# Kernel tuning notes

Hardware: AMD Instinct MI355X
Metric: run time of the kernel (lower is better)

The kernel has to match this reference:

```python
import jax, jax.numpy as jnp
import numpy as np

N_NODES = 100000
AVG_DEG = 32
E_UND = N_NODES * AVG_DEG // 2   # 1.6M undirected edges
E_DIR = 2 * E_UND                # 3.2M directed edges
Q = 4                            # number of communities
NUM_ITER = 10                    # max_num_iter in bp_params


def setup_inputs() -> dict:
    key = jax.random.key(0)
    k1, k2, k3, k4 = jax.random.split(key, 4)
    src_u = jax.random.randint(k1, (E_UND,), 0, N_NODES)
    dst_u = jax.random.randint(k2, (E_UND,), 0, N_NODES)
    # symmetric directed edge list: [forward block | reverse block]
    edge_index = jnp.stack([
        jnp.concatenate([src_u, dst_u]),
        jnp.concatenate([dst_u, src_u]),
    ]).astype(jnp.int64)
    w_u = jax.random.uniform(k3, (E_UND,), dtype=jnp.float32)
    edge_attr = jnp.concatenate([w_u, w_u])  # symmetric weights
    msg_init = jax.random.uniform(k4, (E_DIR, Q), dtype=jnp.float32) + 0.1
    # critical beta for q groups, mean degree c: log(q/(sqrt(c)-1)+1)
    beta = jnp.asarray(np.log(Q / (np.sqrt(AVG_DEG) - 1.0) + 1.0), dtype=jnp.float32)
    return {"edge_index": edge_index, "edge_attr": edge_attr,
            "msg_init": msg_init, "beta": beta, "num_nodes": N_NODES}


def _bp_forward(edge_index, edge_attr, msg_init, beta, num_nodes):
    q = msg_init.shape[1]
    E = edge_index.shape[1]
    e_und = E // 2
    src, dst = edge_index[0], edge_index[1]
    # reverse-edge permutation: edge e <-> e +/- e_und
    rev = jnp.concatenate([jnp.arange(e_und) + e_und, jnp.arange(e_und)])

    two_m = jnp.sum(edge_attr)                                   # = 2m (directed sum)
    deg = jax.ops.segment_sum(edge_attr, src, num_segments=num_nodes)  # weighted degree [N]
    expm1_bw = jnp.expm1(beta * edge_attr)[:, None]              # [E,1]

    psi0 = msg_init / jnp.sum(msg_init, axis=-1, keepdims=True)  # normalized cavity msgs [E,q]
    h0 = jnp.zeros((q,), dtype=msg_init.dtype)                   # external field

    def step(carry, _):
        psi, h = carry
        L = jnp.log1p(psi * expm1_bw)                            # [E,q] log(1 + psi*(e^{bw}-1))
        S = jax.ops.segment_sum(L, dst, num_segments=num_nodes)  # [N,q] incoming log-products
        marg = jax.nn.softmax(h[None, :] + S, axis=-1)           # node marginals [N,q]
        h_new = -(beta / two_m) * jnp.sum(deg[:, None] * marg, axis=0)  # [q]
        # cavity update for edge i->j: all incoming at i except reverse edge j->i
        msg_log = h_new[None, :] + S[src] - L[rev]
        psi_new = jax.nn.softmax(msg_log, axis=-1)
        return (psi_new, h_new), None

    (psi, h), _ = jax.lax.scan(step, (psi0, h0), None, length=NUM_ITER)

    # final node marginals s
    L = jnp.log1p(psi * expm1_bw)
    S = jax.ops.segment_sum(L, dst, num_segments=num_nodes)
    s = jax.nn.softmax(h[None, :] + S, axis=-1)                  # [N,q]

    # modularity: Q = (1/2m) sum_e w_e <s_i, s_j> - sum_t (sum_i d_i s_it / 2m)^2
    link = jnp.sum(edge_attr[:, None] * s[src] * s[dst]) / two_m
    comm_deg = jnp.sum(deg[:, None] * s, axis=0) / two_m         # [q]
    q_mod = link - jnp.sum(comm_deg * comm_deg)
    return s, q_mod


def reference(edge_index, edge_attr, msg_init, beta, num_nodes):
    return _bp_forward(edge_index, edge_attr, msg_init, beta, num_nodes)
```

## Files before the change

kernel.cpp:

```cpp
#include <hip/hip_runtime.h>


#define NBLK 256
#define QD 4
#define SENT 0x7fffffff

__device__ __forceinline__ float wave_red(float v) {
#pragma unroll
  for (int o = 32; o > 0; o >>= 1) v += __shfl_down(v, o, 64);
  return v;
}

__device__ __forceinline__ float4 softmax4(float a, float b, float c, float d) {
  float mx = fmaxf(fmaxf(a, b), fmaxf(c, d));
  float e0 = expf(a - mx), e1 = expf(b - mx), e2 = expf(c - mx), e3 = expf(d - mx);
  float inv = 1.f / (e0 + e1 + e2 + e3);
  return make_float4(e0 * inv, e1 * inv, e2 * inv, e3 * inv);
}

__global__ void hist_rank(const int* __restrict__ ei, int* __restrict__ cnt,
                          int* __restrict__ rank, int E) {
  int G = gridDim.x * blockDim.x;
  int e0 = blockIdx.x * blockDim.x + threadIdx.x;
  int e1 = e0 + G, e2 = e0 + 2 * G, e3 = e0 + 3 * G;
  int d0 = (e0 < E) ? ei[E + e0] : 0;
  int d1 = (e1 < E) ? ei[E + e1] : 0;
  int d2 = (e2 < E) ? ei[E + e2] : 0;
  int d3 = (e3 < E) ? ei[E + e3] : 0;
  if (e0 < E) rank[e0] = atomicAdd(&cnt[d0], 1);
  if (e1 < E) rank[e1] = atomicAdd(&cnt[d1], 1);
  if (e2 < E) rank[e2] = atomicAdd(&cnt[d2], 1);
  if (e3 < E) rank[e3] = atomicAdd(&cnt[d3], 1);
}

__global__ void scanA(const int* __restrict__ cnt, int* __restrict__ out,
                      int* __restrict__ bsum, int N) {
  __shared__ int lds[256];
  int base = blockIdx.x * 1024 + threadIdx.x * 4;
  int v0 = (base + 0 < N) ? cnt[base + 0] : 0;
  int v1 = (base + 1 < N) ? cnt[base + 1] : 0;
  int v2 = (base + 2 < N) ? cnt[base + 2] : 0;
  int v3 = (base + 3 < N) ? cnt[base + 3] : 0;
  lds[threadIdx.x] = v0 + v1 + v2 + v3;
  __syncthreads();
  for (int off = 1; off < 256; off <<= 1) {
    int x = (threadIdx.x >= off) ? lds[threadIdx.x - off] : 0;
    __syncthreads();
    if (threadIdx.x >= off) lds[threadIdx.x] += x;
    __syncthreads();
  }
  int excl = (threadIdx.x == 0) ? 0 : lds[threadIdx.x - 1];
  if (threadIdx.x == 255) bsum[blockIdx.x] = lds[255];
  if (base + 0 < N) out[base + 0] = excl;
  if (base + 1 < N) out[base + 1] = excl + v0;
  if (base + 2 < N) out[base + 2] = excl + v0 + v1;
  if (base + 3 < N) out[base + 3] = excl + v0 + v1 + v2;
}

__global__ void scanB(int* __restrict__ bsum, int NB) {
  __shared__ int lds[256];
  int v = (threadIdx.x < NB) ? bsum[threadIdx.x] : 0;
  lds[threadIdx.x] = v;
  __syncthreads();
  for (int off = 1; off < 256; off <<= 1) {
    int x = (threadIdx.x >= off) ? lds[threadIdx.x - off] : 0;
    __syncthreads();
    if (threadIdx.x >= off) lds[threadIdx.x] += x;
    __syncthreads();
  }
  int excl = (threadIdx.x == 0) ? 0 : lds[threadIdx.x - 1];
  if (threadIdx.x < NB) bsum[threadIdx.x] = excl;
}

__global__ void scanC(int* __restrict__ rowStart, const int* __restrict__ bsum,
                      int N, int E) {
  int i = blockIdx.x * blockDim.x + threadIdx.x;
  if (i < N) rowStart[i] += bsum[i >> 10];
  if (i == 0) rowStart[N] = E;
}

__global__ void scatter_inc(const int* __restrict__ ei, const int* __restrict__ rowStart,
                            const int* __restrict__ rank, int* __restrict__ inc, int E) {
  int e = blockIdx.x * blockDim.x + threadIdx.x;
  if (e >= E) return;
  int d = ei[E + e];
  inc[rowStart[d] + rank[e]] = e;
}

__global__ void build_nodeOf(const int* __restrict__ rowStart, int* __restrict__ nodeOf,
                             int N) {
  int n = blockIdx.x * blockDim.x + threadIdx.x;
  if (n >= N) return;
  int s = rowStart[n], e = rowStart[n + 1];
  for (int k = s; k < e; ++k) nodeOf[k] = n;
}

__global__ void reduce_w(const float* __restrict__ w, double* __restrict__ two_m, int E) {
  __shared__ float blk[4];
  int G = gridDim.x * blockDim.x;
  float acc = 0.f;
  for (int i = blockIdx.x * blockDim.x + threadIdx.x; i < E; i += G) acc += w[i];
  acc = wave_red(acc);
  int wid = threadIdx.x >> 6;
  if ((threadIdx.x & 63) == 0) blk[wid] = acc;
  __syncthreads();
  if (threadIdx.x == 0)
    atomicAdd(two_m, (double)(blk[0] + blk[1] + blk[2] + blk[3]));
}

__global__ void setup_pairs(const float* __restrict__ w, const float* __restrict__ msg,
                            const float* __restrict__ beta_p, float* __restrict__ L,
                            float* __restrict__ em_buf, int Eh) {
  int t = blockIdx.x * blockDim.x + threadIdx.x;
  if (t >= Eh) return;
  float beta = beta_p[0];
  float wv = w[t];
  float em = expm1f(beta * wv);
  em_buf[t] = em;
  float4 m1 = *reinterpret_cast<const float4*>(&msg[(size_t)t * QD]);
  float4 m2 = *reinterpret_cast<const float4*>(&msg[((size_t)t + Eh) * QD]);
  float i1 = 1.f / (m1.x + m1.y + m1.z + m1.w);
  float i2 = 1.f / (m2.x + m2.y + m2.z + m2.w);
  float4 L1 = make_float4(log1pf(m1.x * i1 * em), log1pf(m1.y * i1 * em),
                          log1pf(m1.z * i1 * em), log1pf(m1.w * i1 * em));
  float4 L2 = make_float4(log1pf(m2.x * i2 * em), log1pf(m2.y * i2 * em),
                          log1pf(m2.z * i2 * em), log1pf(m2.w * i2 * em));
  *reinterpret_cast<float4*>(&L[(size_t)t * QD]) = L1;
  *reinterpret_cast<float4*>(&L[((size_t)t + Eh) * QD]) = L2;
}

template <int NC>
__global__ void gather_seg(const int* __restrict__ inc, const int* __restrict__ nodeOf,
                           const float* __restrict__ src, float* __restrict__ out,
                           int E) {
  const int lane = threadIdx.x & 63;
  const int wid = threadIdx.x >> 6;
  const long long base = ((long long)blockIdx.x * (blockDim.x >> 6) + wid) * 256;
  if (base >= E) return;
  int n[4], idx[4];
  float v[4][NC];
#pragma unroll
  for (int w = 0; w < 4; ++w) {
    long long k = base + w * 64 + lane;
    n[w] = (k < E) ? nodeOf[k] : SENT;
    idx[w] = (k < E) ? inc[k] : 0;
  }
#pragma unroll
  for (int w = 0; w < 4; ++w) {
    long long k = base + w * 64 + lane;
    if (k < E) {
      if constexpr (NC == 4) {
        float4 t = *reinterpret_cast<const float4*>(&src[(size_t)idx[w] * 4]);
        v[w][0] = t.x; v[w][1] = t.y; v[w][2] = t.z; v[w][3] = t.w;
      } else {
        v[w][0] = src[idx[w]];
      }
    } else {
#pragma unroll
      for (int c = 0; c < NC; ++c) v[w][c] = 0.f;
    }
  }
  int n00 = __shfl(n[0], 0, 64);
  int prevn = (base > 0) ? nodeOf[base - 1] : -1;
  const int incomplete = (prevn == n00) ? n00 : -1;
  int nwf[4];
#pragma unroll
  for (int w = 0; w < 3; ++w) nwf[w] = __shfl(n[w + 1], 0, 64);
  nwf[3] = (base + 256 < E) ? nodeOf[base + 256] : -1;

  float cv[NC];
#pragma unroll
  for (int c = 0; c < NC; ++c) cv[c] = 0.f;
  int cn = -1;
#pragma unroll
  for (int w = 0; w < 4; ++w) {
    int nn = n[w];
#pragma unroll
    for (int d = 1; d < 64; d <<= 1) {
      int pn = __shfl_up(nn, d, 64);
      float pv[NC];
#pragma unroll
      for (int c = 0; c < NC; ++c) pv[c] = __shfl_up(v[w][c], d, 64);
      if (lane >= d && pn == nn) {
#pragma unroll
        for (int c = 0; c < NC; ++c) v[w][c] += pv[c];
      }
    }
    if (nn == cn) {
#pragma unroll
      for (int c = 0; c < NC; ++c) v[w][c] += cv[c];
    }
    int nnext = __shfl_down(nn, 1, 64);
    if (lane == 63) nnext = nwf[w];
    bool segend = (nn != SENT) && (nnext != nn);
    if (segend) {
      if (nn == incomplete) {
#pragma unroll
        for (int c = 0; c < NC; ++c) atomicAdd(&out[(size_t)nn * NC + c], v[w][c]);
      } else {
        if constexpr (NC == 4) {
          *reinterpret_cast<float4*>(&out[(size_t)nn * 4]) =
              make_float4(v[w][0], v[w][1], v[w][2], v[w][3]);
        } else {
          out[nn] = v[w][0];
        }
      }
    }
    int last_n = __shfl(nn, 63, 64);
    float lv[NC];
#pragma unroll
    for (int c = 0; c < NC; ++c) lv[c] = __shfl(v[w][c], 63, 64);
    bool last_end = (nwf[w] != last_n) || (last_n == SENT);
    if (last_end) {
      cn = -1;
#pragma unroll
      for (int c = 0; c < NC; ++c) cv[c] = 0.f;
    } else {
      cn = last_n;
#pragma unroll
      for (int c = 0; c < NC; ++c) cv[c] = lv[c];
    }
  }
  if (cn != -1 && lane == 0) {
#pragma unroll
    for (int c = 0; c < NC; ++c) atomicAdd(&out[(size_t)cn * NC + c], cv[c]);
  }
}

__global__ void node_post(const float* __restrict__ S, const float* __restrict__ deg,
                          const double* __restrict__ hsum_prev, double* __restrict__ hsum_new,
                          const float* __restrict__ beta_p, const double* __restrict__ two_m,
                          int N) {
  __shared__ float blk[4][4];
  int n = blockIdx.x * blockDim.x + threadIdx.x;
  float scale = -beta_p[0] / (float)two_m[0];
  float h0 = scale * (float)hsum_prev[0];
  float h1 = scale * (float)hsum_prev[1];
  float h2 = scale * (float)hsum_prev[2];
  float h3 = scale * (float)hsum_prev[3];
  float a0 = 0.f, a1 = 0.f, a2 = 0.f, a3 = 0.f;
  if (n < N) {
    float4 Sv = *reinterpret_cast<const float4*>(&S[(size_t)n * QD]);
    float4 p = softmax4(h0 + Sv.x, h1 + Sv.y, h2 + Sv.z, h3 + Sv.w);
    float d = deg[n];
    a0 = d * p.x; a1 = d * p.y; a2 = d * p.z; a3 = d * p.w;
  }
  a0 = wave_red(a0); a1 = wave_red(a1); a2 = wave_red(a2); a3 = wave_red(a3);
  int wid = threadIdx.x >> 6;
  if ((threadIdx.x & 63) == 0) {
    blk[wid][0] = a0; blk[wid][1] = a1; blk[wid][2] = a2; blk[wid][3] = a3;
  }
  __syncthreads();
  if (threadIdx.x < 4) {
    float s = blk[0][threadIdx.x] + blk[1][threadIdx.x] + blk[2][threadIdx.x] +
              blk[3][threadIdx.x];
    atomicAdd(&hsum_new[threadIdx.x], (double)s);
  }
}

__global__ void node_post_final(const float* __restrict__ S, const float* __restrict__ deg,
                                const double* __restrict__ hsum, const float* __restrict__ beta_p,
                                const double* __restrict__ two_m, float* __restrict__ out_s,
                                double* __restrict__ comm_raw, int N) {
  __shared__ float blk[4][4];
  int n = blockIdx.x * blockDim.x + threadIdx.x;
  float scale = -beta_p[0] / (float)two_m[0];
  float h0 = scale * (float)hsum[0];
  float h1 = scale * (float)hsum[1];
  float h2 = scale * (float)hsum[2];
  float h3 = scale * (float)hsum[3];
  float a0 = 0.f, a1 = 0.f, a2 = 0.f, a3 = 0.f;
  if (n < N) {
    float4 Sv = *reinterpret_cast<const float4*>(&S[(size_t)n * QD]);
    float4 p = softmax4(h0 + Sv.x, h1 + Sv.y, h2 + Sv.z, h3 + Sv.w);
    *reinterpret_cast<float4*>(&out_s[(size_t)n * QD]) = p;
    float d = deg[n];
    a0 = d * p.x; a1 = d * p.y; a2 = d * p.z; a3 = d * p.w;
  }
  a0 = wave_red(a0); a1 = wave_red(a1); a2 = wave_red(a2); a3 = wave_red(a3);
  int wid = threadIdx.x >> 6;
  if ((threadIdx.x & 63) == 0) {
    blk[wid][0] = a0; blk[wid][1] = a1; blk[wid][2] = a2; blk[wid][3] = a3;
  }
  __syncthreads();
  if (threadIdx.x < 4) {
    float s = blk[0][threadIdx.x] + blk[1][threadIdx.x] + blk[2][threadIdx.x] +
              blk[3][threadIdx.x];
    atomicAdd(&comm_raw[threadIdx.x], (double)s);
  }
}

__global__ void edge_step(const int* __restrict__ ei, const float* __restrict__ em_buf,
                          const float* __restrict__ S, float* __restrict__ L,
                          const double* __restrict__ hsum, const float* __restrict__ beta_p,
                          const double* __restrict__ two_m, int E, int Eh) {
  int t = blockIdx.x * blockDim.x + threadIdx.x;
  if (t >= Eh) return;
  float scale = -beta_p[0] / (float)two_m[0];
  float h0 = scale * (float)hsum[0];
  float h1 = scale * (float)hsum[1];
  float h2 = scale * (float)hsum[2];
  float h3 = scale * (float)hsum[3];
  int s1 = ei[t];
  int d1 = ei[E + t];
  float em = em_buf[t];
  float4 L1 = *reinterpret_cast<const float4*>(&L[(size_t)t * QD]);
  float4 L2 = *reinterpret_cast<const float4*>(&L[((size_t)t + Eh) * QD]);
  float4 Ss = *reinterpret_cast<const float4*>(&S[(size_t)s1 * QD]);
  float4 Sd = *reinterpret_cast<const float4*>(&S[(size_t)d1 * QD]);
  float4 p1 = softmax4(h0 + Ss.x - L2.x, h1 + Ss.y - L2.y,
                       h2 + Ss.z - L2.z, h3 + Ss.w - L2.w);
  float4 p2 = softmax4(h0 + Sd.x - L1.x, h1 + Sd.y - L1.y,
                       h2 + Sd.z - L1.z, h3 + Sd.w - L1.w);
  float4 n1 = make_float4(log1pf(p1.x * em), log1pf(p1.y * em),
                          log1pf(p1.z * em), log1pf(p1.w * em));
  float4 n2 = make_float4(log1pf(p2.x * em), log1pf(p2.y * em),
                          log1pf(p2.z * em), log1pf(p2.w * em));
  *reinterpret_cast<float4*>(&L[(size_t)t * QD]) = n1;
  *reinterpret_cast<float4*>(&L[((size_t)t + Eh) * QD]) = n2;
}

__global__ void edge_final(const int* __restrict__ ei, const float* __restrict__ w,
                           const float* __restrict__ out_s,
                           double* __restrict__ link_raw, int E, int Eh) {
  __shared__ float blk[4];
  int G = gridDim.x * blockDim.x;
  float c = 0.f;
  for (int t = blockIdx.x * blockDim.x + threadIdx.x; t < Eh; t += G) {
    int s1 = ei[t];
    int d1 = ei[E + t];
    float4 a = *reinterpret_cast<const float4*>(&out_s[(size_t)s1 * QD]);
    float4 b = *reinterpret_cast<const float4*>(&out_s[(size_t)d1 * QD]);
    float dot = a.x * b.x + a.y * b.y + a.z * b.z + a.w * b.w;
    c += 2.f * w[t] * dot;
  }
  c = wave_red(c);
  int wid = threadIdx.x >> 6;
  if ((threadIdx.x & 63) == 0) blk[wid] = c;
  __syncthreads();
  if (threadIdx.x == 0)
    atomicAdd(link_raw, (double)(blk[0] + blk[1] + blk[2] + blk[3]));
}

__global__ void finalize(const double* __restrict__ scal, float* __restrict__ out_q) {
  double tm = scal[0];
  double link = scal[1] / tm;
  double acc = 0.0;
#pragma unroll
  for (int k = 0; k < QD; ++k) {
    double c = scal[2 + k] / tm;
    acc += c * c;
  }
  out_q[0] = (float)(link - acc);
}

extern "C" void kernel_launch(void* const* d_in, const int* in_sizes, int n_in,
                              void* d_out, int out_size, void* d_ws, size_t ws_size,
                              hipStream_t stream) {
  const int* ei = (const int*)d_in[0];
  const float* w = (const float*)d_in[1];
  const float* msg = (const float*)d_in[2];
  const float* beta_p = (const float*)d_in[3];

  const int E = in_sizes[1];
  const int Eh = E / 2;
  const int N = (out_size - 1) / QD;

  char* p = (char*)d_ws;
  double* scal = (double*)p;
  size_t off = 512;
  int* cnt = (int*)(p + off); off += (size_t)N * 4;
  int* rowStart = (int*)(p + off); off += (size_t)(N + 1) * 4;
  off = (off + 127) & ~(size_t)127;
  int* bsum = (int*)(p + off); off += 1024;
  int* inc = (int*)(p + off); off += (size_t)E * 4;
  float* deg = (float*)(p + off); off += (size_t)N * 4;
  off = (off + 15) & ~(size_t)15;
  float* S = (float*)(p + off); off += (size_t)N * QD * 4;
  float* em = (float*)(p + off); off += (size_t)Eh * 4;
  off = (off + 15) & ~(size_t)15;
  float* L = (float*)(p + off); off += (size_t)E * QD * 4;
  int* rank = (int*)L;
  int* nodeOf = (int*)(p + off); off += (size_t)E * 4;
  (void)ws_size;

  double* hs = scal + 6;
  const int gEdir = (E + NBLK - 1) / NBLK;
  const int gE = (Eh + NBLK - 1) / NBLK;
  const int gN = (N + NBLK - 1) / NBLK;
  const int gH = (E + NBLK * 4 - 1) / (NBLK * 4);
  const int gW = (E + 1023) / 1024;
  const int NBscan = (N + 1023) / 1024;

  hipMemsetAsync(scal, 0, 512, stream);
  hipMemsetAsync(cnt, 0, (size_t)N * 4, stream);
  hipMemsetAsync(deg, 0, (size_t)N * 4, stream);

  hist_rank<<<gH, NBLK, 0, stream>>>(ei, cnt, rank, E);
  scanA<<<NBscan, 256, 0, stream>>>(cnt, rowStart, bsum, N);
  scanB<<<1, 256, 0, stream>>>(bsum, NBscan);
  scanC<<<(N + NBLK) / NBLK, NBLK, 0, stream>>>(rowStart, bsum, N, E);
  scatter_inc<<<gEdir, NBLK, 0, stream>>>(ei, rowStart, rank, inc, E);
  build_nodeOf<<<gN, NBLK, 0, stream>>>(rowStart, nodeOf, N);

  reduce_w<<<256, NBLK, 0, stream>>>(w, scal, E);
  setup_pairs<<<gE, NBLK, 0, stream>>>(w, msg, beta_p, L, em, Eh);
  gather_seg<1><<<gW, NBLK, 0, stream>>>(inc, nodeOf, w, deg, E);

  float* out_s = (float*)d_out;
  for (int i = 1; i <= 10; ++i) {
    hipMemsetAsync(S, 0, (size_t)N * QD * 4, stream);
    gather_seg<4><<<gW, NBLK, 0, stream>>>(inc, nodeOf, L, S, E);
    node_post<<<gN, NBLK, 0, stream>>>(S, deg, hs + 4 * (i - 1), hs + 4 * i,
                                       beta_p, scal, N);
    edge_step<<<gE, NBLK, 0, stream>>>(ei, em, S, L, hs + 4 * i, beta_p, scal, E, Eh);
  }
  hipMemsetAsync(S, 0, (size_t)N * QD * 4, stream);
  gather_seg<4><<<gW, NBLK, 0, stream>>>(inc, nodeOf, L, S, E);
  node_post_final<<<gN, NBLK, 0, stream>>>(S, deg, hs + 40, beta_p, scal,
                                           out_s, scal + 2, N);
  edge_final<<<512, NBLK, 0, stream>>>(ei, w, out_s, scal + 1, E, Eh);
  finalize<<<1, 1, 0, stream>>>(scal, out_s + (size_t)N * QD);
}
```

Measured before the change: 1.797 ms.

## Switch BP messages from log domain to product domain with segmented products

```diff
diff --git a/kernel.cpp b/kernel.cpp
--- a/kernel.cpp
+++ b/kernel.cpp
@@ -11,26 +11,27 @@
   return v;
 }
 
-__device__ __forceinline__ float4 softmax4(float a, float b, float c, float d) {
-  float mx = fmaxf(fmaxf(a, b), fmaxf(c, d));
-  float e0 = expf(a - mx), e1 = expf(b - mx), e2 = expf(c - mx), e3 = expf(d - mx);
-  float inv = 1.f / (e0 + e1 + e2 + e3);
-  return make_float4(e0 * inv, e1 * inv, e2 * inv, e3 * inv);
+__device__ __forceinline__ void atomicMulF(float* addr, float val) {
+  unsigned int old = __float_as_uint(*addr), assumed;
+  do {
+    assumed = old;
+    float nv = __uint_as_float(assumed) * val;
+    old = atomicCAS((unsigned int*)addr, assumed, __float_as_uint(nv));
+  } while (old != assumed);
 }
 
 __global__ void hist_rank(const int* __restrict__ ei, int* __restrict__ cnt,
                           int* __restrict__ rank, int E) {
   int G = gridDim.x * blockDim.x;
-  int e0 = blockIdx.x * blockDim.x + threadIdx.x;
-  int e1 = e0 + G, e2 = e0 + 2 * G, e3 = e0 + 3 * G;
-  int d0 = (e0 < E) ? ei[E + e0] : 0;
-  int d1 = (e1 < E) ? ei[E + e1] : 0;
-  int d2 = (e2 < E) ? ei[E + e2] : 0;
-  int d3 = (e3 < E) ? ei[E + e3] : 0;
-  if (e0 < E) rank[e0] = atomicAdd(&cnt[d0], 1);
-  if (e1 < E) rank[e1] = atomicAdd(&cnt[d1], 1);
-  if (e2 < E) rank[e2] = atomicAdd(&cnt[d2], 1);
-  if (e3 < E) rank[e3] = atomicAdd(&cnt[d3], 1);
+  int e[8], d[8];
+#pragma unroll
+  for (int j = 0; j < 8; ++j) {
+    e[j] = blockIdx.x * blockDim.x + threadIdx.x + j * G;
+    d[j] = (e[j] < E) ? ei[E + e[j]] : 0;
+  }
+#pragma unroll
+  for (int j = 0; j < 8; ++j)
+    if (e[j] < E) rank[e[j]] = atomicAdd(&cnt[d[j]], 1);
 }
 
 __global__ void scanA(const int* __restrict__ cnt, int* __restrict__ out,
@@ -81,10 +82,15 @@
 
 __global__ void scatter_inc(const int* __restrict__ ei, const int* __restrict__ rowStart,
                             const int* __restrict__ rank, int* __restrict__ inc, int E) {
-  int e = blockIdx.x * blockDim.x + threadIdx.x;
-  if (e >= E) return;
-  int d = ei[E + e];
-  inc[rowStart[d] + rank[e]] = e;
+  int G = gridDim.x * blockDim.x;
+#pragma unroll
+  for (int j = 0; j < 4; ++j) {
+    int e = blockIdx.x * blockDim.x + threadIdx.x + j * G;
+    if (e < E) {
+      int d = ei[E + e];
+      inc[rowStart[d] + rank[e]] = e;
+    }
+  }
 }
 
 __global__ void build_nodeOf(const int* __restrict__ rowStart, int* __restrict__ nodeOf,
@@ -95,58 +101,62 @@
   for (int k = s; k < e; ++k) nodeOf[k] = n;
 }
 
-__global__ void reduce_w(const float* __restrict__ w, double* __restrict__ two_m, int E) {
+__global__ void setup_pairs(const float* __restrict__ w, const float* __restrict__ msg,
+                            const float* __restrict__ beta_p, float* __restrict__ F,
+                            float* __restrict__ em_buf, double* __restrict__ two_m,
+                            int Eh) {
   __shared__ float blk[4];
-  int G = gridDim.x * blockDim.x;
-  float acc = 0.f;
-  for (int i = blockIdx.x * blockDim.x + threadIdx.x; i < E; i += G) acc += w[i];
-  acc = wave_red(acc);
+  int t = blockIdx.x * blockDim.x + threadIdx.x;
+  float tw = 0.f;
+  if (t < Eh) {
+    float beta = beta_p[0];
+    float wv = w[t];
+    tw = 2.f * wv;
+    float em = expm1f(beta * wv);
+    em_buf[t] = em;
+    float4 m1 = *reinterpret_cast<const float4*>(&msg[(size_t)t * QD]);
+    float4 m2 = *reinterpret_cast<const float4*>(&msg[((size_t)t + Eh) * QD]);
+    float i1 = em / (m1.x + m1.y + m1.z + m1.w);
+    float i2 = em / (m2.x + m2.y + m2.z + m2.w);
+    float4 F1 = make_float4(fmaf(m1.x, i1, 1.f), fmaf(m1.y, i1, 1.f),
+                            fmaf(m1.z, i1, 1.f), fmaf(m1.w, i1, 1.f));
+    float4 F2 = make_float4(fmaf(m2.x, i2, 1.f), fmaf(m2.y, i2, 1.f),
+                            fmaf(m2.z, i2, 1.f), fmaf(m2.w, i2, 1.f));
+    *reinterpret_cast<float4*>(&F[(size_t)t * QD]) = F1;
+    *reinterpret_cast<float4*>(&F[((size_t)t + Eh) * QD]) = F2;
+  }
+  tw = wave_red(tw);
   int wid = threadIdx.x >> 6;
-  if ((threadIdx.x & 63) == 0) blk[wid] = acc;
+  if ((threadIdx.x & 63) == 0) blk[wid] = tw;
   __syncthreads();
   if (threadIdx.x == 0)
     atomicAdd(two_m, (double)(blk[0] + blk[1] + blk[2] + blk[3]));
 }
 
-__global__ void setup_pairs(const float* __restrict__ w, const float* __restrict__ msg,
-                            const float* __restrict__ beta_p, float* __restrict__ L,
-                            float* __restrict__ em_buf, int Eh) {
-  int t = blockIdx.x * blockDim.x + threadIdx.x;
-  if (t >= Eh) return;
-  float beta = beta_p[0];
-  float wv = w[t];
-  float em = expm1f(beta * wv);
-  em_buf[t] = em;
-  float4 m1 = *reinterpret_cast<const float4*>(&msg[(size_t)t * QD]);
-  float4 m2 = *reinterpret_cast<const float4*>(&msg[((size_t)t + Eh) * QD]);
-  float i1 = 1.f / (m1.x + m1.y + m1.z + m1.w);
-  float i2 = 1.f / (m2.x + m2.y + m2.z + m2.w);
-  float4 L1 = make_float4(log1pf(m1.x * i1 * em), log1pf(m1.y * i1 * em),
-                          log1pf(m1.z * i1 * em), log1pf(m1.w * i1 * em));
-  float4 L2 = make_float4(log1pf(m2.x * i2 * em), log1pf(m2.y * i2 * em),
-                          log1pf(m2.z * i2 * em), log1pf(m2.w * i2 * em));
-  *reinterpret_cast<float4*>(&L[(size_t)t * QD]) = L1;
-  *reinterpret_cast<float4*>(&L[((size_t)t + Eh) * QD]) = L2;
-}
-
-template <int NC>
+__global__ void fillP(float* __restrict__ P, int n4) {
+  int i = blockIdx.x * blockDim.x + threadIdx.x;
+  if (i < n4) P[i] = 1.0f;
+}
+
+template <int NC, bool PROD, int NW>
 __global__ void gather_seg(const int* __restrict__ inc, const int* __restrict__ nodeOf,
                            const float* __restrict__ src, float* __restrict__ out,
                            int E) {
   const int lane = threadIdx.x & 63;
   const int wid = threadIdx.x >> 6;
-  const long long base = ((long long)blockIdx.x * (blockDim.x >> 6) + wid) * 256;
+  const long long base = ((long long)blockIdx.x * (blockDim.x >> 6) + wid) * (NW * 64);
   if (base >= E) return;
-  int n[4], idx[4];
-  float v[4][NC];
-#pragma unroll
-  for (int w = 0; w < 4; ++w) {
+  const float IDENT = PROD ? 1.f : 0.f;
+  int n[NW], idx[NW];
+  float v[NW][NC];
+#pragma unroll
+  for (int w = 0; w < NW; ++w) {
     long long k = base + w * 64 + lane;
     n[w] = (k < E) ? nodeOf[k] : SENT;
     idx[w] = (k < E) ? inc[k] : 0;
   }
 #pragma unroll
-  for (int w = 0; w < 4; ++w) {
+  for (int w = 0; w < NW; ++w) {
     long long k = base + w * 64 + lane;
     if (k < E) {
       if constexpr (NC == 4) {
@@ -157,23 +167,23 @@
       }
     } else {
 #pragma unroll
-      for (int c = 0; c < NC; ++c) v[w][c] = 0.f;
+      for (int c = 0; c < NC; ++c) v[w][c] = IDENT;
     }
   }
   int n00 = __shfl(n[0], 0, 64);
   int prevn = (base > 0) ? nodeOf[base - 1] : -1;
   const int incomplete = (prevn == n00) ? n00 : -1;
-  int nwf[4];
-#pragma unroll
-  for (int w = 0; w < 3; ++w) nwf[w] = __shfl(n[w + 1], 0, 64);
-  nwf[3] = (base + 256 < E) ? nodeOf[base + 256] : -1;
+  int nwf[NW];
+#pragma unroll
+  for (int w = 0; w < NW - 1; ++w) nwf[w] = __shfl(n[w + 1], 0, 64);
+  nwf[NW - 1] = (base + NW * 64 < E) ? nodeOf[base + NW * 64] : -1;
 
   float cv[NC];
 #pragma unroll
-  for (int c = 0; c < NC; ++c) cv[c] = 0.f;
+  for (int c = 0; c < NC; ++c) cv[c] = IDENT;
   int cn = -1;
 #pragma unroll
-  for (int w = 0; w < 4; ++w) {
+  for (int w = 0; w < NW; ++w) {
     int nn = n[w];
 #pragma unroll
     for (int d = 1; d < 64; d <<= 1) {
@@ -183,12 +193,16 @@
       for (int c = 0; c < NC; ++c) pv[c] = __shfl_up(v[w][c], d, 64);
       if (lane >= d && pn == nn) {
 #pragma unroll
-        for (int c = 0; c < NC; ++c) v[w][c] += pv[c];
+        for (int c = 0; c < NC; ++c) {
+          if constexpr (PROD) v[w][c] *= pv[c]; else v[w][c] += pv[c];
+        }
       }
     }
     if (nn == cn) {
 #pragma unroll
-      for (int c = 0; c < NC; ++c) v[w][c] += cv[c];
+      for (int c = 0; c < NC; ++c) {
+        if constexpr (PROD) v[w][c] *= cv[c]; else v[w][c] += cv[c];
+      }
     }
     int nnext = __shfl_down(nn, 1, 64);
     if (lane == 63) nnext = nwf[w];
@@ -196,7 +210,10 @@
     if (segend) {
       if (nn == incomplete) {
 #pragma unroll
-        for (int c = 0; c < NC; ++c) atomicAdd(&out[(size_t)nn * NC + c], v[w][c]);
+        for (int c = 0; c < NC; ++c) {
+          if constexpr (PROD) atomicMulF(&out[(size_t)nn * NC + c], v[w][c]);
+          else atomicAdd(&out[(size_t)nn * NC + c], v[w][c]);
+        }
       } else {
         if constexpr (NC == 4) {
           *reinterpret_cast<float4*>(&out[(size_t)nn * 4]) =
@@ -214,7 +231,7 @@
     if (last_end) {
       cn = -1;
 #pragma unroll
-      for (int c = 0; c < NC; ++c) cv[c] = 0.f;
+      for (int c = 0; c < NC; ++c) cv[c] = IDENT;
     } else {
       cn = last_n;
 #pragma unroll
@@ -223,27 +240,30 @@
   }
   if (cn != -1 && lane == 0) {
 #pragma unroll
-    for (int c = 0; c < NC; ++c) atomicAdd(&out[(size_t)cn * NC + c], cv[c]);
-  }
-}
-
-__global__ void node_post(const float* __restrict__ S, const float* __restrict__ deg,
+    for (int c = 0; c < NC; ++c) {
+      if constexpr (PROD) atomicMulF(&out[(size_t)cn * NC + c], cv[c]);
+      else atomicAdd(&out[(size_t)cn * NC + c], cv[c]);
+    }
+  }
+}
+
+__global__ void node_post(const float* __restrict__ P, const float* __restrict__ deg,
                           const double* __restrict__ hsum_prev, double* __restrict__ hsum_new,
                           const float* __restrict__ beta_p, const double* __restrict__ two_m,
                           int N) {
   __shared__ float blk[4][4];
   int n = blockIdx.x * blockDim.x + threadIdx.x;
   float scale = -beta_p[0] / (float)two_m[0];
-  float h0 = scale * (float)hsum_prev[0];
-  float h1 = scale * (float)hsum_prev[1];
-  float h2 = scale * (float)hsum_prev[2];
-  float h3 = scale * (float)hsum_prev[3];
+  float e0 = expf(scale * (float)hsum_prev[0]);
+  float e1 = expf(scale * (float)hsum_prev[1]);
+  float e2 = expf(scale * (float)hsum_prev[2]);
+  float e3 = expf(scale * (float)hsum_prev[3]);
   float a0 = 0.f, a1 = 0.f, a2 = 0.f, a3 = 0.f;
   if (n < N) {
-    float4 Sv = *reinterpret_cast<const float4*>(&S[(size_t)n * QD]);
-    float4 p = softmax4(h0 + Sv.x, h1 + Sv.y, h2 + Sv.z, h3 + Sv.w);
-    float d = deg[n];
-    a0 = d * p.x; a1 = d * p.y; a2 = d * p.z; a3 = d * p.w;
+    float4 Pv = *reinterpret_cast<const float4*>(&P[(size_t)n * QD]);
+    float m0 = e0 * Pv.x, m1 = e1 * Pv.y, m2 = e2 * Pv.z, m3 = e3 * Pv.w;
+    float dinv = deg[n] / (m0 + m1 + m2 + m3);
+    a0 = m0 * dinv; a1 = m1 * dinv; a2 = m2 * dinv; a3 = m3 * dinv;
   }
   a0 = wave_red(a0); a1 = wave_red(a1); a2 = wave_red(a2); a3 = wave_red(a3);
   int wid = threadIdx.x >> 6;
@@ -258,24 +278,26 @@
   }
 }
 
-__global__ void node_post_final(const float* __restrict__ S, const float* __restrict__ deg,
+__global__ void node_post_final(const float* __restrict__ P, const float* __restrict__ deg,
                                 const double* __restrict__ hsum, const float* __restrict__ beta_p,
                                 const double* __restrict__ two_m, float* __restrict__ out_s,
                                 double* __restrict__ comm_raw, int N) {
   __shared__ float blk[4][4];
   int n = blockIdx.x * blockDim.x + threadIdx.x;
   float scale = -beta_p[0] / (float)two_m[0];
-  float h0 = scale * (float)hsum[0];
-  float h1 = scale * (float)hsum[1];
-  float h2 = scale * (float)hsum[2];
-  float h3 = scale * (float)hsum[3];
+  float e0 = expf(scale * (float)hsum[0]);
+  float e1 = expf(scale * (float)hsum[1]);
+  float e2 = expf(scale * (float)hsum[2]);
+  float e3 = expf(scale * (float)hsum[3]);
   float a0 = 0.f, a1 = 0.f, a2 = 0.f, a3 = 0.f;
   if (n < N) {
-    float4 Sv = *reinterpret_cast<const float4*>(&S[(size_t)n * QD]);
-    float4 p = softmax4(h0 + Sv.x, h1 + Sv.y, h2 + Sv.z, h3 + Sv.w);
-    *reinterpret_cast<float4*>(&out_s[(size_t)n * QD]) = p;
+    float4 Pv = *reinterpret_cast<const float4*>(&P[(size_t)n * QD]);
+    float m0 = e0 * Pv.x, m1 = e1 * Pv.y, m2 = e2 * Pv.z, m3 = e3 * Pv.w;
+    float inv = 1.f / (m0 + m1 + m2 + m3);
+    float4 s = make_float4(m0 * inv, m1 * inv, m2 * inv, m3 * inv);
+    *reinterpret_cast<float4*>(&out_s[(size_t)n * QD]) = s;
     float d = deg[n];
-    a0 = d * p.x; a1 = d * p.y; a2 = d * p.z; a3 = d * p.w;
+    a0 = d * s.x; a1 = d * s.y; a2 = d * s.z; a3 = d * s.w;
   }
   a0 = wave_red(a0); a1 = wave_red(a1); a2 = wave_red(a2); a3 = wave_red(a3);
   int wid = threadIdx.x >> 6;
@@ -290,34 +312,44 @@
   }
 }
 
-__global__ void edge_step(const int* __restrict__ ei, const float* __restrict__ em_buf,
-                          const float* __restrict__ S, float* __restrict__ L,
+__global__ void edge_fuse(const int* __restrict__ ei, const float* __restrict__ em_buf,
+                          const float* __restrict__ P, float* __restrict__ F,
                           const double* __restrict__ hsum, const float* __restrict__ beta_p,
                           const double* __restrict__ two_m, int E, int Eh) {
   int t = blockIdx.x * blockDim.x + threadIdx.x;
   if (t >= Eh) return;
   float scale = -beta_p[0] / (float)two_m[0];
-  float h0 = scale * (float)hsum[0];
-  float h1 = scale * (float)hsum[1];
-  float h2 = scale * (float)hsum[2];
-  float h3 = scale * (float)hsum[3];
+  float e0 = expf(scale * (float)hsum[0]);
+  float e1 = expf(scale * (float)hsum[1]);
+  float e2 = expf(scale * (float)hsum[2]);
+  float e3 = expf(scale * (float)hsum[3]);
   int s1 = ei[t];
   int d1 = ei[E + t];
   float em = em_buf[t];
-  float4 L1 = *reinterpret_cast<const float4*>(&L[(size_t)t * QD]);
-  float4 L2 = *reinterpret_cast<const float4*>(&L[((size_t)t + Eh) * QD]);
-  float4 Ss = *reinterpret_cast<const float4*>(&S[(size_t)s1 * QD]);
-  float4 Sd = *reinterpret_cast<const float4*>(&S[(size_t)d1 * QD]);
-  float4 p1 = softmax4(h0 + Ss.x - L2.x, h1 + Ss.y - L2.y,
-                       h2 + Ss.z - L2.z, h3 + Ss.w - L2.w);
-  float4 p2 = softmax4(h0 + Sd.x - L1.x, h1 + Sd.y - L1.y,
-                       h2 + Sd.z - L1.z, h3 + Sd.w - L1.w);
-  float4 n1 = make_float4(log1pf(p1.x * em), log1pf(p1.y * em),
-                          log1pf(p1.z * em), log1pf(p1.w * em));
-  float4 n2 = make_float4(log1pf(p2.x * em), log1pf(p2.y * em),
-                          log1pf(p2.z * em), log1pf(p2.w * em));
-  *reinterpret_cast<float4*>(&L[(size_t)t * QD]) = n1;
-  *reinterpret_cast<float4*>(&L[((size_t)t + Eh) * QD]) = n2;
+  float4 F1 = *reinterpret_cast<const float4*>(&F[(size_t)t * QD]);
+  float4 F2 = *reinterpret_cast<const float4*>(&F[((size_t)t + Eh) * QD]);
+  float4 Ps = *reinterpret_cast<const float4*>(&P[(size_t)s1 * QD]);
+  float4 Pd = *reinterpret_cast<const float4*>(&P[(size_t)d1 * QD]);
+  {
+    float a01 = F2.x * F2.y, a23 = F2.z * F2.w;
+    float x0 = F2.y * a23, x1 = F2.x * a23, x2 = a01 * F2.w, x3 = a01 * F2.z;
+    float n0 = e0 * Ps.x * x0, n1 = e1 * Ps.y * x1;
+    float n2 = e2 * Ps.z * x2, n3 = e3 * Ps.w * x3;
+    float tt = em / (n0 + n1 + n2 + n3);
+    float4 Fn = make_float4(fmaf(n0, tt, 1.f), fmaf(n1, tt, 1.f),
+                            fmaf(n2, tt, 1.f), fmaf(n3, tt, 1.f));
+    *reinterpret_cast<float4*>(&F[(size_t)t * QD]) = Fn;
+  }
+  {
+    float a01 = F1.x * F1.y, a23 = F1.z * F1.w;
+    float x0 = F1.y * a23, x1 = F1.x * a23, x2 = a01 * F1.w, x3 = a01 * F1.z;
+    float n0 = e0 * Pd.x * x0, n1 = e1 * Pd.y * x1;
+    float n2 = e2 * Pd.z * x2, n3 = e3 * Pd.w * x3;
+    float tt = em / (n0 + n1 + n2 + n3);
+    float4 Fn = make_float4(fmaf(n0, tt, 1.f), fmaf(n1, tt, 1.f),
+                            fmaf(n2, tt, 1.f), fmaf(n3, tt, 1.f));
+    *reinterpret_cast<float4*>(&F[((size_t)t + Eh) * QD]) = Fn;
+  }
 }
 
 __global__ void edge_final(const int* __restrict__ ei, const float* __restrict__ w,
@@ -376,11 +408,11 @@
   int* inc = (int*)(p + off); off += (size_t)E * 4;
   float* deg = (float*)(p + off); off += (size_t)N * 4;
   off = (off + 15) & ~(size_t)15;
-  float* S = (float*)(p + off); off += (size_t)N * QD * 4;
+  float* P = (float*)(p + off); off += (size_t)N * QD * 4;
   float* em = (float*)(p + off); off += (size_t)Eh * 4;
   off = (off + 15) & ~(size_t)15;
-  float* L = (float*)(p + off); off += (size_t)E * QD * 4;
-  int* rank = (int*)L;
+  float* F = (float*)(p + off); off += (size_t)E * QD * 4;
+  int* rank = (int*)F;
   int* nodeOf = (int*)(p + off); off += (size_t)E * 4;
   (void)ws_size;
 
@@ -388,8 +420,11 @@
   const int gEdir = (E + NBLK - 1) / NBLK;
   const int gE = (Eh + NBLK - 1) / NBLK;
   const int gN = (N + NBLK - 1) / NBLK;
-  const int gH = (E + NBLK * 4 - 1) / (NBLK * 4);
-  const int gW = (E + 1023) / 1024;
+  const int gH = (E + NBLK * 8 - 1) / (NBLK * 8);
+  const int gSc = (E + NBLK * 4 - 1) / (NBLK * 4);
+  const int gWp = (E + 2047) / 2048;
+  const int gWd = (E + 1023) / 1024;
+  const int gF = (4 * N + NBLK - 1) / NBLK;
   const int NBscan = (N + 1023) / 1024;
 
   hipMemsetAsync(scal, 0, 512, stream);
@@ -400,24 +435,23 @@
   scanA<<<NBscan, 256, 0, stream>>>(cnt, rowStart, bsum, N);
   scanB<<<1, 256, 0, stream>>>(bsum, NBscan);
   scanC<<<(N + NBLK) / NBLK, NBLK, 0, stream>>>(rowStart, bsum, N, E);
-  scatter_inc<<<gEdir, NBLK, 0, stream>>>(ei, rowStart, rank, inc, E);
+  scatter_inc<<<gSc, NBLK, 0, stream>>>(ei, rowStart, rank, inc, E);
   build_nodeOf<<<gN, NBLK, 0, stream>>>(rowStart, nodeOf, N);
 
-  reduce_w<<<256, NBLK, 0, stream>>>(w, scal, E);
-  setup_pairs<<<gE, NBLK, 0, stream>>>(w, msg, beta_p, L, em, Eh);
-  gather_seg<1><<<gW, NBLK, 0, stream>>>(inc, nodeOf, w, deg, E);
+  setup_pairs<<<gE, NBLK, 0, stream>>>(w, msg, beta_p, F, em, scal, Eh);
+  gather_seg<1, false, 4><<<gWd, NBLK, 0, stream>>>(inc, nodeOf, w, deg, E);
 
   float* out_s = (float*)d_out;
   for (int i = 1; i <= 10; ++i) {
-    hipMemsetAsync(S, 0, (size_t)N * QD * 4, stream);
-    gather_seg<4><<<gW, NBLK, 0, stream>>>(inc, nodeOf, L, S, E);
-    node_post<<<gN, NBLK, 0, stream>>>(S, deg, hs + 4 * (i - 1), hs + 4 * i,
+    fillP<<<gF, NBLK, 0, stream>>>(P, 4 * N);
+    gather_seg<4, true, 8><<<gWp, NBLK, 0, stream>>>(inc, nodeOf, F, P, E);
+    node_post<<<gN, NBLK, 0, stream>>>(P, deg, hs + 4 * (i - 1), hs + 4 * i,
                                        beta_p, scal, N);
-    edge_step<<<gE, NBLK, 0, stream>>>(ei, em, S, L, hs + 4 * i, beta_p, scal, E, Eh);
-  }
-  hipMemsetAsync(S, 0, (size_t)N * QD * 4, stream);
-  gather_seg<4><<<gW, NBLK, 0, stream>>>(inc, nodeOf, L, S, E);
-  node_post_final<<<gN, NBLK, 0, stream>>>(S, deg, hs + 40, beta_p, scal,
+    edge_fuse<<<gE, NBLK, 0, stream>>>(ei, em, P, F, hs + 4 * i, beta_p, scal, E, Eh);
+  }
+  fillP<<<gF, NBLK, 0, stream>>>(P, 4 * N);
+  gather_seg<4, true, 8><<<gWp, NBLK, 0, stream>>>(inc, nodeOf, F, P, E);
+  node_post_final<<<gN, NBLK, 0, stream>>>(P, deg, hs + 40, beta_p, scal,
                                            out_s, scal + 2, N);
   edge_final<<<512, NBLK, 0, stream>>>(ei, w, out_s, scal + 1, E, Eh);
   finalize<<<1, 1, 0, stream>>>(scal, out_s + (size_t)N * QD);
```

Result: faster. 1.719 ms (-4.3%).
